# Optimization experiments

Measured on AMD Instinct MI355X. Metric: run time of the kernel, lower is better.

## Reference

```python
import jax, jax.numpy as jnp
import numpy as np

N = 100_000      # total nodes in batched graph
NE = 800_000     # total edges
G = 1_000        # number of graphs in batch
V_DIM = 128      # node feat dim (== H_DIM, required by GRUCell usage)
E_DIM = 64       # edge feat dim
H_DIM = 128      # hidden dim
K_HEAD = 4       # multi-scale interaction heads


def _leaky(x):
    return jnp.where(x >= 0, x, 0.1 * x)


def _gru_cell(x, h, Wih, Whh, bih, bhh):
    # torch nn.GRUCell math; Wih/Whh stored as [in, 3*h] with (r,z,n) chunk order
    gi = x @ Wih + bih
    gh = h @ Whh + bhh
    ir, iz, inn = jnp.split(gi, 3, axis=-1)
    hr, hz, hn = jnp.split(gh, 3, axis=-1)
    r = jax.nn.sigmoid(ir + hr)
    z = jax.nn.sigmoid(iz + hz)
    n = jnp.tanh(inn + r * hn)
    return (1.0 - z) * n + z * h


def setup_inputs() -> dict:
    key = jax.random.key(0)
    ks = iter(jax.random.split(key, 48))
    def rn(shape, scale=0.05):
        return (jax.random.normal(next(ks), shape) * scale).astype(jnp.float32)
    inp = {}
    inp["v"] = rn((N, V_DIM), 1.0)
    inp["e"] = rn((NE, E_DIM), 1.0)
    inp["s"] = rn((G, V_DIM), 1.0)
    inp["edge_src"] = jax.random.randint(next(ks), (NE,), 0, N)
    inp["edge_dst"] = jax.random.randint(next(ks), (NE,), 0, N)
    inp["node_graph"] = jnp.repeat(jnp.arange(G), N // G)  # sorted segment ids
    # top-level linears (stored [in, out])
    inp["A_w"] = rn((V_DIM, H_DIM)); inp["A_b"] = rn((H_DIM,))
    inp["mA_w"] = rn((K_HEAD, V_DIM, H_DIM)); inp["mA_b"] = rn((K_HEAD, H_DIM))
    inp["mB_w"] = rn((K_HEAD, V_DIM, H_DIM)); inp["mB_b"] = rn((K_HEAD, H_DIM))
    inp["mC_w"] = rn((K_HEAD, H_DIM)); inp["mC_b"] = rn((K_HEAD,))
    inp["mD_w"] = rn((K_HEAD, V_DIM, H_DIM)); inp["mD_b"] = rn((K_HEAD, H_DIM))
    inp["B_w"] = rn((H_DIM * K_HEAD, H_DIM)); inp["B_b"] = rn((H_DIM,))
    inp["C_w"] = rn((V_DIM, H_DIM)); inp["C_b"] = rn((H_DIM,))
    inp["K_w"] = rn((E_DIM, H_DIM)); inp["K_b"] = rn((H_DIM,))
    inp["E_w"] = rn((H_DIM + V_DIM, H_DIM)); inp["E_b"] = rn((H_DIM,))
    for pfx in ("gm", "gs"):
        inp[pfx + "_A_w"] = rn((H_DIM, H_DIM)); inp[pfx + "_A_b"] = rn((H_DIM,))
        inp[pfx + "_B_w"] = rn((H_DIM, H_DIM)); inp[pfx + "_B_b"] = rn((H_DIM,))
        inp[pfx + "_Wih"] = rn((H_DIM, 3 * H_DIM)); inp[pfx + "_Whh"] = rn((H_DIM, 3 * H_DIM))
        inp[pfx + "_bih"] = rn((3 * H_DIM,)); inp[pfx + "_bhh"] = rn((3 * H_DIM,))
    return inp


def reference(v, e, s, edge_src, edge_dst, node_graph,
              A_w, A_b, mA_w, mA_b, mB_w, mB_b, mC_w, mC_b, mD_w, mD_b,
              B_w, B_b, C_w, C_b, K_w, K_b, E_w, E_b,
              gm_A_w, gm_A_b, gm_B_w, gm_B_b, gm_Wih, gm_Whh, gm_bih, gm_bhh,
              gs_A_w, gs_A_b, gs_B_w, gs_B_b, gs_Wih, gs_Whh, gs_bih, gs_bhh):
    # super -> super
    s2s = jnp.tanh(s @ A_w + A_b)                                       # [G,H]
    # multi-head node->super attention pooling (Multi_scale_interaction)
    d_node = jnp.tanh(jnp.einsum('nv,kvh->knh', v, mA_w) + mA_b[:, None, :])     # [K,N,H]
    d_super = jnp.tanh(jnp.einsum('gv,kvh->kgh', s, mB_w) + mB_b[:, None, :])    # [K,G,H]
    a = jnp.einsum('knh,kh->nk', d_node * d_super[:, node_graph, :], mC_w) + mC_b[None, :]  # [N,K]
    a_max = jax.ops.segment_max(a, node_graph, num_segments=G, indices_are_sorted=True)
    a_exp = jnp.exp(a - a_max[node_graph])
    denom = jax.ops.segment_sum(a_exp, node_graph, num_segments=G, indices_are_sorted=True)
    attn = a_exp / denom[node_graph]                                    # per-graph softmax, [N,K]
    d_v = jnp.einsum('nv,kvh->nkh', v, mD_w) + mD_b[None, :, :]         # [N,K,H]
    pooled = jax.ops.segment_sum(d_v * attn[:, :, None], node_graph, num_segments=G,
                                 indices_are_sorted=True)               # [G,K,H]
    m2s = jnp.tanh(pooled.reshape(G, K_HEAD * H_DIM) @ B_w + B_b)       # [G,H]
    # super -> node broadcast
    s2m = jnp.tanh(s @ C_w + C_b)[node_graph]                           # [N,H]
    # edge-wise message: leaky_relu(K(e) * v_src) summed into destination node
    ve = _leaky((e @ K_w + K_b) * v[edge_src])                          # [E,H]
    sve = jax.ops.segment_sum(ve, edge_dst, num_segments=N)             # [N,H]
    m2m = _leaky(jnp.concatenate([sve, v], axis=1) @ E_w + E_b)         # [N,H]
    # adaptive GRU gate: node update
    z_m = jax.nn.sigmoid(m2m @ gm_A_w + gm_A_b + s2m @ gm_B_w + gm_B_b)
    h_m = z_m * s2m + (1.0 - z_m) * m2m
    update_v = _gru_cell(v, h_m, gm_Wih, gm_Whh, gm_bih, gm_bhh)
    # adaptive GRU gate: supernode update
    z_s = jax.nn.sigmoid(s2s @ gs_A_w + gs_A_b + m2s @ gs_B_w + gs_B_b)
    h_s = z_s * m2s + (1.0 - z_s) * s2s
    update_s = _gru_cell(s, h_s, gs_Wih, gs_Whh, gs_bih, gs_bhh)
    return (update_v, update_s)
```

## Files before the change

kernel.cpp:

```cpp
#include <hip/hip_runtime.h>

#define NN   100000
#define NEDG 800000
#define NG   1000
#define HD   128
#define EDIM 64

typedef unsigned short u16;
typedef __bf16 bf16x8 __attribute__((ext_vector_type(8)));
typedef float f32x4 __attribute__((ext_vector_type(4)));

#define MFMA16(a, b, c) __builtin_amdgcn_mfma_f32_16x16x32_bf16(a, b, c, 0, 0, 0)

#define WS_E    0
#define WS_GA   4096
#define WS_WIH  6144
#define WS_WHH  12288
#define WS_MA0  18432
#define WS_KW   26624
#define WS_LANES 27648

#define BF(base, NTT, ks, nt, lane) \
    (*(const bf16x8*)(wsw + (size_t)((base) + (((ks) * (NTT) + (nt)) * 64 + (lane))) * 8))

__device__ __forceinline__ float sigmoidf_(float x) { return 1.0f / (1.0f + __expf(-x)); }
__device__ __forceinline__ float tanhf_(float x) {
    float ax = fabsf(x);
    float e  = __expf(-2.0f * ax);
    float t  = (1.0f - e) / (1.0f + e);
    return copysignf(t, x);
}
__device__ __forceinline__ float leaky_(float x) { return x >= 0.f ? x : 0.1f * x; }
__device__ __forceinline__ u16 f2bf(float x) {
    union { float f; unsigned u; } c; c.f = x;
    unsigned r = c.u + 0x7FFF + ((c.u >> 16) & 1);
    return (u16)(r >> 16);
}

__device__ __forceinline__ void stg4(u16* lds, int P, int r, int c0, float4 v4) {
    int byteoff = (c0 << 1) ^ ((r & 7) << 4);
    u16* p = lds + r * P + (byteoff >> 1);
    p[0] = f2bf(v4.x); p[1] = f2bf(v4.y); p[2] = f2bf(v4.z); p[3] = f2bf(v4.w);
}
__device__ __forceinline__ void stg1(u16* lds, int P, int r, int c, u16 val) {
    int byteoff = (c << 1) ^ ((r & 7) << 4);
    lds[r * P + (byteoff >> 1)] = val;
}
__device__ __forceinline__ bf16x8 ldA(const u16* lds, int P, int r, int ks, int hi) {
    int byteoff = (ks * 64 + (hi << 4)) ^ ((r & 7) << 4);
    return *(const bf16x8*)(lds + r * P + (byteoff >> 1));
}

__global__ __launch_bounds__(256) void wconv(
    const float* __restrict__ E_w, const float* __restrict__ gmA_w,
    const float* __restrict__ Wih, const float* __restrict__ Whh,
    const float* __restrict__ mA_w, const float* __restrict__ K_w,
    u16* __restrict__ dst)
{
    int t = blockIdx.x * 256 + threadIdx.x;
    if (t >= WS_LANES) return;
    const float* W; int N; int local;
    if (t < 4096)       { W = E_w;  N = 128; local = t; }
    else if (t < 6144)  { W = gmA_w; N = 128; local = t - 4096; }
    else if (t < 12288) { W = Wih;  N = 384; local = t - 6144; }
    else if (t < 18432) { W = Whh;  N = 384; local = t - 12288; }
    else if (t < 26624) { int k = (t - 18432) >> 11; W = mA_w + k * 128 * 128; N = 128; local = (t - 18432) & 2047; }
    else                { W = K_w;  N = 128; local = t - 26624; }
    int lane = local & 63;
    int fid  = local >> 6;
    int NT = N >> 4;
    int ks = fid / NT, nt = fid - ks * NT;
    int krow = ks * 32 + ((lane >> 4) << 3);
    int col  = nt * 16 + (lane & 15);
    u16* d = dst + (size_t)t * 8;
    #pragma unroll
    for (int j = 0; j < 8; j++) d[j] = f2bf(W[(size_t)(krow + j) * N + col]);
}

__global__ __launch_bounds__(256) void k_hist(const int* __restrict__ edst, int* __restrict__ cnt) {
    int i = blockIdx.x * 256 + threadIdx.x;
    if (i < NEDG) atomicAdd(&cnt[edst[i]], 1);
}

__global__ __launch_bounds__(256) void k_scan1(const int* __restrict__ cnt,
                                               int* __restrict__ excl, int* __restrict__ bsum) {
    __shared__ int sd[256];
    int t = threadIdx.x, b = blockIdx.x;
    int base = b * 1024 + t * 4;
    int v0 = (base + 0 < NN) ? cnt[base + 0] : 0;
    int v1 = (base + 1 < NN) ? cnt[base + 1] : 0;
    int v2 = (base + 2 < NN) ? cnt[base + 2] : 0;
    int v3 = (base + 3 < NN) ? cnt[base + 3] : 0;
    int s = v0 + v1 + v2 + v3;
    sd[t] = s;
    __syncthreads();
    for (int off = 1; off < 256; off <<= 1) {
        int x = (t >= off) ? sd[t - off] : 0;
        __syncthreads();
        sd[t] += x;
        __syncthreads();
    }
    int incl = sd[t];
    int ex = incl - s;
    if (base + 0 < NN) excl[base + 0] = ex;
    if (base + 1 < NN) excl[base + 1] = ex + v0;
    if (base + 2 < NN) excl[base + 2] = ex + v0 + v1;
    if (base + 3 < NN) excl[base + 3] = ex + v0 + v1 + v2;
    if (t == 255) bsum[b] = incl;
}

#define NSCB 98
__global__ void k_scan2(int* __restrict__ bsum) {
    if (threadIdx.x == 0 && blockIdx.x == 0) {
        int run = 0;
        for (int i = 0; i < NSCB; i++) { int t = bsum[i]; bsum[i] = run; run += t; }
    }
}

__global__ __launch_bounds__(256) void k_scan3(const int* __restrict__ excl,
                                               const int* __restrict__ bsum, int* __restrict__ start) {
    int i = blockIdx.x * 256 + threadIdx.x;
    if (i < NN) start[i] = excl[i] + bsum[i >> 10];
}

__global__ __launch_bounds__(256) void k_scatter(const int* __restrict__ edst,
                                                 int* __restrict__ start, int* __restrict__ perm) {
    int i = blockIdx.x * 256 + threadIdx.x;
    if (i < NEDG) {
        int pos = atomicAdd(&start[edst[i]], 1);
        perm[pos] = i;
    }
}

__global__ __launch_bounds__(128) void k1_graph(
    const float* __restrict__ s,
    const float* __restrict__ A_w, const float* __restrict__ A_b,
    const float* __restrict__ mB_w, const float* __restrict__ mB_b,
    const float* __restrict__ mC_w,
    const float* __restrict__ C_w, const float* __restrict__ C_b,
    const float* __restrict__ gmB_w, const float* __restrict__ gmA_b, const float* __restrict__ gmB_b,
    float* __restrict__ s2s, float* __restrict__ wkg,
    float* __restrict__ s2m_tab, float* __restrict__ t2)
{
    __shared__ float sm[HD];
    __shared__ float sm2[HD];
    const int g = blockIdx.x, t = threadIdx.x;
    sm[t] = s[g * HD + t];
    __syncthreads();
    {
        float a = 0.f;
        #pragma unroll 8
        for (int i = 0; i < HD; i++) a = fmaf(sm[i], A_w[i * HD + t], a);
        s2s[g * HD + t] = tanhf_(a + A_b[t]);
    }
    for (int k = 0; k < 4; k++) {
        float a = 0.f;
        const float* W = mB_w + k * HD * HD;
        #pragma unroll 8
        for (int i = 0; i < HD; i++) a = fmaf(sm[i], W[i * HD + t], a);
        float d = tanhf_(a + mB_b[k * HD + t]);
        wkg[(k * NG + g) * HD + t] = d * mC_w[k * HD + t];
    }
    float s2m;
    {
        float a = 0.f;
        #pragma unroll 8
        for (int i = 0; i < HD; i++) a = fmaf(sm[i], C_w[i * HD + t], a);
        s2m = tanhf_(a + C_b[t]);
        s2m_tab[g * HD + t] = s2m;
    }
    sm2[t] = s2m;
    __syncthreads();
    {
        float a = 0.f;
        #pragma unroll 8
        for (int i = 0; i < HD; i++) a = fmaf(sm2[i], gmB_w[i * HD + t], a);
        t2[g * HD + t] = a + gmA_b[t] + gmB_b[t];
    }
}

__global__ __launch_bounds__(256) void k2_ascore(
    const float* __restrict__ v, const int* __restrict__ ngr,
    const u16* __restrict__ wsw,
    const float* __restrict__ mA_b, const float* __restrict__ mC_b,
    const float* __restrict__ wkg,
    float* __restrict__ aexp, float* __restrict__ denom)
{
    __shared__ u16 VT[64 * 128];
    const int tid = threadIdx.x;
    const int n0 = blockIdx.x * 64;
    #pragma unroll
    for (int l = 0; l < 8; l++) {
        int i = tid + 256 * l;
        int r = i >> 5, c0 = (i & 31) << 2;
        int node = n0 + r;
        float4 vv = (node < NN) ? *(const float4*)(v + (size_t)node * HD + c0)
                                : make_float4(0.f, 0.f, 0.f, 0.f);
        stg4(VT, 128, r, c0, vv);
    }
    __syncthreads();
    const int lane = tid & 63, w = tid >> 6;
    const int l15 = lane & 15, hi = lane >> 4;
    const int rbase = w * 16;
    bf16x8 av[4];
    #pragma unroll
    for (int ks = 0; ks < 4; ks++) av[ks] = ldA(VT, 128, rbase + l15, ks, hi);
    int gq[4], nodeq[4];
    #pragma unroll
    for (int q = 0; q < 4; q++) {
        int nd = n0 + rbase + hi * 4 + q;
        nodeq[q] = nd;
        gq[q] = ngr[min(nd, NN - 1)];
    }
    for (int k = 0; k < 4; k++) {
        float rs[4] = {0.f, 0.f, 0.f, 0.f};
        const float* bias = mA_b + k * HD;
        #pragma unroll
        for (int nt = 0; nt < 8; nt++) {
            f32x4 acc = {0.f, 0.f, 0.f, 0.f};
            #pragma unroll
            for (int ks = 0; ks < 4; ks++)
                acc = MFMA16(av[ks], BF(WS_MA0 + k * 2048, 8, ks, nt, lane), acc);
            int col = nt * 16 + l15;
            float bb = bias[col];
            #pragma unroll
            for (int q = 0; q < 4; q++)
                rs[q] += tanhf_(acc[q] + bb) * wkg[((size_t)k * NG + gq[q]) * HD + col];
        }
        #pragma unroll
        for (int q = 0; q < 4; q++) {
            float x = rs[q];
            x += __shfl_xor(x, 1); x += __shfl_xor(x, 2);
            x += __shfl_xor(x, 4); x += __shfl_xor(x, 8);
            if (l15 == 0 && nodeq[q] < NN) {
                float ev = __expf(x + mC_b[k]);
                aexp[(size_t)nodeq[q] * 4 + k] = ev;
                atomicAdd(&denom[gq[q] * 4 + k], ev);
            }
        }
    }
}

__global__ __launch_bounds__(256) void k3_edge_sorted(
    const float* __restrict__ e, const float* __restrict__ v,
    const int* __restrict__ esrc, const int* __restrict__ edst,
    const int* __restrict__ perm,
    const u16* __restrict__ wsw, const float* __restrict__ K_b,
    float* __restrict__ sve)
{
    __shared__ u16 ET[64 * 64];
    __shared__ int pid[64];
    const int tid = threadIdx.x;
    const int e0 = blockIdx.x * 64;
    if (tid < 64) pid[tid] = perm[e0 + tid];
    __syncthreads();
    #pragma unroll
    for (int l = 0; l < 4; l++) {
        int i = tid + 256 * l;
        int r = i >> 4, c0 = (i & 15) << 2;
        float4 ev4 = *(const float4*)(e + (size_t)pid[r] * EDIM + c0);
        stg4(ET, 64, r, c0, ev4);
    }
    __syncthreads();
    const int lane = tid & 63, w = tid >> 6;
    const int l15 = lane & 15, hi = lane >> 4;
    const int rbase = w * 16;
    bf16x8 ae[2];
    #pragma unroll
    for (int ks = 0; ks < 2; ks++) ae[ks] = ldA(ET, 64, rbase + l15, ks, hi);
    int sq[4], dq[4];
    #pragma unroll
    for (int q = 0; q < 4; q++) {
        int ei = pid[rbase + hi * 4 + q];
        sq[q] = esrc[ei]; dq[q] = edst[ei];
    }
    #pragma unroll
    for (int nt = 0; nt < 8; nt++) {
        f32x4 acc = {0.f, 0.f, 0.f, 0.f};
        acc = MFMA16(ae[0], BF(WS_KW, 8, 0, nt, lane), acc);
        acc = MFMA16(ae[1], BF(WS_KW, 8, 1, nt, lane), acc);
        int col = nt * 16 + l15;
        float kb = K_b[col];
        float vals[4];
        #pragma unroll
        for (int q = 0; q < 4; q++)
            vals[q] = leaky_((acc[q] + kb) * v[(size_t)sq[q] * HD + col]);
        float a = vals[0];
        #pragma unroll
        for (int q = 1; q < 4; q++) {
            if (dq[q] == dq[q - 1]) a += vals[q];
            else { atomicAdd(&sve[(size_t)dq[q - 1] * HD + col], a); a = vals[q]; }
        }
        atomicAdd(&sve[(size_t)dq[3] * HD + col], a);
    }
}

__global__ __launch_bounds__(256) void k3_edge_unsorted(
    const float* __restrict__ e, const float* __restrict__ v,
    const int* __restrict__ esrc, const int* __restrict__ edst,
    const u16* __restrict__ wsw, const float* __restrict__ K_b,
    float* __restrict__ sve)
{
    __shared__ u16 ET[64 * 64];
    const int tid = threadIdx.x;
    const int e0 = blockIdx.x * 64;
    #pragma unroll
    for (int l = 0; l < 4; l++) {
        int i = tid + 256 * l;
        int r = i >> 4, c0 = (i & 15) << 2;
        float4 ev4 = *(const float4*)(e + (size_t)(e0 + r) * EDIM + c0);
        stg4(ET, 64, r, c0, ev4);
    }
    __syncthreads();
    const int lane = tid & 63, w = tid >> 6;
    const int l15 = lane & 15, hi = lane >> 4;
    const int rbase = w * 16;
    bf16x8 ae[2];
    #pragma unroll
    for (int ks = 0; ks < 2; ks++) ae[ks] = ldA(ET, 64, rbase + l15, ks, hi);
    int sq[4], dq[4];
    #pragma unroll
    for (int q = 0; q < 4; q++) {
        int ei = e0 + rbase + hi * 4 + q;
        sq[q] = esrc[ei]; dq[q] = edst[ei];
    }
    #pragma unroll
    for (int nt = 0; nt < 8; nt++) {
        f32x4 acc = {0.f, 0.f, 0.f, 0.f};
        acc = MFMA16(ae[0], BF(WS_KW, 8, 0, nt, lane), acc);
        acc = MFMA16(ae[1], BF(WS_KW, 8, 1, nt, lane), acc);
        int col = nt * 16 + l15;
        float kb = K_b[col];
        #pragma unroll
        for (int q = 0; q < 4; q++) {
            float val = leaky_((acc[q] + kb) * v[(size_t)sq[q] * HD + col]);
            atomicAdd(&sve[(size_t)dq[q] * HD + col], val);
        }
    }
}

__global__ __launch_bounds__(256) void k4_vbar(
    const float* __restrict__ v, const int* __restrict__ ngr,
    const float* __restrict__ aexp, const float* __restrict__ denom,
    float* __restrict__ vbar)
{
    const int tid = threadIdx.x;
    const int d = tid & 127;
    const int hf = tid >> 7;
    const int n0 = blockIdx.x * 32 + hf * 16;
    int gcur = -1;
    float a0 = 0.f, a1 = 0.f, a2 = 0.f, a3 = 0.f;
    float4 rd = make_float4(0.f, 0.f, 0.f, 0.f);
    for (int nd = 0; nd < 16; nd++) {
        int n = n0 + nd;
        int g = ngr[n];
        if (g != gcur) {
            if (gcur >= 0) {
                atomicAdd(&vbar[(gcur * 4 + 0) * HD + d], a0);
                atomicAdd(&vbar[(gcur * 4 + 1) * HD + d], a1);
                atomicAdd(&vbar[(gcur * 4 + 2) * HD + d], a2);
                atomicAdd(&vbar[(gcur * 4 + 3) * HD + d], a3);
                a0 = a1 = a2 = a3 = 0.f;
            }
            float4 dn = *(const float4*)&denom[g * 4];
            rd = make_float4(1.f / dn.x, 1.f / dn.y, 1.f / dn.z, 1.f / dn.w);
            gcur = g;
        }
        float4 ae = *(const float4*)&aexp[n * 4];
        float vv = v[(size_t)n * HD + d];
        a0 = fmaf(ae.x * rd.x, vv, a0);
        a1 = fmaf(ae.y * rd.y, vv, a1);
        a2 = fmaf(ae.z * rd.z, vv, a2);
        a3 = fmaf(ae.w * rd.w, vv, a3);
    }
    atomicAdd(&vbar[(gcur * 4 + 0) * HD + d], a0);
    atomicAdd(&vbar[(gcur * 4 + 1) * HD + d], a1);
    atomicAdd(&vbar[(gcur * 4 + 2) * HD + d], a2);
    atomicAdd(&vbar[(gcur * 4 + 3) * HD + d], a3);
}

__global__ __launch_bounds__(128) void k5_super(
    const float* __restrict__ s, const float* __restrict__ vbar,
    const float* __restrict__ mD_w, const float* __restrict__ mD_b,
    const float* __restrict__ B_w, const float* __restrict__ B_b,
    const float* __restrict__ s2s,
    const float* __restrict__ gsA_w, const float* __restrict__ gsA_b,
    const float* __restrict__ gsB_w, const float* __restrict__ gsB_b,
    const float* __restrict__ gsWih, const float* __restrict__ gsWhh,
    const float* __restrict__ gsbih, const float* __restrict__ gsbhh,
    float* __restrict__ out_s)
{
    __shared__ float vb[4 * HD];
    __shared__ float p[4 * HD];
    __shared__ float m2s_l[HD];
    __shared__ float s2s_l[HD];
    __shared__ float hs_l[HD];
    __shared__ float srow[HD];
    const int g = blockIdx.x, t = threadIdx.x;
    #pragma unroll
    for (int l = 0; l < 4; l++) vb[t + HD * l] = vbar[(size_t)g * 4 * HD + t + HD * l];
    srow[t]  = s[g * HD + t];
    s2s_l[t] = s2s[g * HD + t];
    __syncthreads();
    for (int k = 0; k < 4; k++) {
        float a = 0.f;
        const float* W = mD_w + k * HD * HD;
        #pragma unroll 8
        for (int i = 0; i < HD; i++) a = fmaf(vb[k * HD + i], W[i * HD + t], a);
        p[k * HD + t] = a + mD_b[k * HD + t];
    }
    __syncthreads();
    float m2s;
    {
        float a = 0.f;
        #pragma unroll 8
        for (int j = 0; j < 4 * HD; j++) a = fmaf(p[j], B_w[j * HD + t], a);
        m2s = tanhf_(a + B_b[t]);
        m2s_l[t] = m2s;
    }
    __syncthreads();
    float hs;
    {
        float za = 0.f, zb = 0.f;
        #pragma unroll 8
        for (int i = 0; i < HD; i++) {
            za = fmaf(s2s_l[i], gsA_w[i * HD + t], za);
            zb = fmaf(m2s_l[i], gsB_w[i * HD + t], zb);
        }
        float z = sigmoidf_(za + gsA_b[t] + zb + gsB_b[t]);
        hs = z * m2s + (1.f - z) * s2s_l[t];
        hs_l[t] = hs;
    }
    __syncthreads();
    float gi0 = 0.f, gh0 = 0.f, gi1 = 0.f, gh1 = 0.f, gi2 = 0.f, gh2 = 0.f;
    #pragma unroll 4
    for (int i = 0; i < HD; i++) {
        float sv = srow[i], hv = hs_l[i];
        gi0 = fmaf(sv, gsWih[i * 384 + t], gi0);
        gh0 = fmaf(hv, gsWhh[i * 384 + t], gh0);
        gi1 = fmaf(sv, gsWih[i * 384 + 128 + t], gi1);
        gh1 = fmaf(hv, gsWhh[i * 384 + 128 + t], gh1);
        gi2 = fmaf(sv, gsWih[i * 384 + 256 + t], gi2);
        gh2 = fmaf(hv, gsWhh[i * 384 + 256 + t], gh2);
    }
    float r  = sigmoidf_(gi0 + gsbih[t] + gh0 + gsbhh[t]);
    float z2 = sigmoidf_(gi1 + gsbih[128 + t] + gh1 + gsbhh[128 + t]);
    float nn = tanhf_(gi2 + gsbih[256 + t] + r * (gh2 + gsbhh[256 + t]));
    out_s[g * HD + t] = (1.f - z2) * nn + z2 * hs;
}

__global__ __launch_bounds__(256) void k6_node(
    const float* __restrict__ v, const int* __restrict__ ngr,
    const float* __restrict__ sve, const u16* __restrict__ wsw,
    const float* __restrict__ E_b,
    const float* __restrict__ s2m_tab, const float* __restrict__ t2,
    const float* __restrict__ bih, const float* __restrict__ bhh,
    float* __restrict__ out_v)
{
    __shared__ u16 VT[64 * 128];
    __shared__ u16 ST[64 * 128];
    __shared__ u16 XT[64 * 128];
    const int tid = threadIdx.x;
    const int n0 = blockIdx.x * 64;
    #pragma unroll
    for (int l = 0; l < 8; l++) {
        int i = tid + 256 * l;
        int r = i >> 5, c0 = (i & 31) << 2;
        int node = n0 + r;
        float4 a = (node < NN) ? *(const float4*)(v   + (size_t)node * HD + c0) : make_float4(0.f, 0.f, 0.f, 0.f);
        float4 b = (node < NN) ? *(const float4*)(sve + (size_t)node * HD + c0) : make_float4(0.f, 0.f, 0.f, 0.f);
        stg4(VT, 128, r, c0, a);
        stg4(ST, 128, r, c0, b);
    }
    __syncthreads();
    const int lane = tid & 63, w = tid >> 6;
    const int l15 = lane & 15, hi = lane >> 4;
    const int rbase = w * 16;
    bf16x8 av[4], ax[4];
    #pragma unroll
    for (int ks = 0; ks < 4; ks++) {
        av[ks] = ldA(VT, 128, rbase + l15, ks, hi);
        ax[ks] = ldA(ST, 128, rbase + l15, ks, hi);
    }
    int gq[4], nodeq[4];
    #pragma unroll
    for (int q = 0; q < 4; q++) {
        int nd = n0 + rbase + hi * 4 + q;
        nodeq[q] = nd;
        gq[q] = ngr[min(nd, NN - 1)];
    }
    f32x4 hmf[8];
    #pragma unroll
    for (int nt = 0; nt < 8; nt++) {
        f32x4 acc = {0.f, 0.f, 0.f, 0.f};
        #pragma unroll
        for (int ks = 0; ks < 4; ks++) acc = MFMA16(ax[ks], BF(WS_E, 8, ks, nt, lane), acc);
        #pragma unroll
        for (int ks = 0; ks < 4; ks++) acc = MFMA16(av[ks], BF(WS_E, 8, 4 + ks, nt, lane), acc);
        int col = nt * 16 + l15;
        float eb = E_b[col];
        f32x4 m;
        #pragma unroll
        for (int q = 0; q < 4; q++) m[q] = leaky_(acc[q] + eb);
        hmf[nt] = m;
    }
    #pragma unroll
    for (int nt = 0; nt < 8; nt++) {
        int col = nt * 16 + l15;
        #pragma unroll
        for (int q = 0; q < 4; q++) stg1(ST, 128, rbase + hi * 4 + q, col, f2bf(hmf[nt][q]));
    }
    bf16x8 am[4];
    #pragma unroll
    for (int ks = 0; ks < 4; ks++) am[ks] = ldA(ST, 128, rbase + l15, ks, hi);
    #pragma unroll
    for (int nt = 0; nt < 8; nt++) {
        f32x4 acc = {0.f, 0.f, 0.f, 0.f};
        #pragma unroll
        for (int ks = 0; ks < 4; ks++) acc = MFMA16(am[ks], BF(WS_GA, 8, ks, nt, lane), acc);
        int col = nt * 16 + l15;
        #pragma unroll
        for (int q = 0; q < 4; q++) {
            int g = gq[q];
            float z  = sigmoidf_(acc[q] + t2[(size_t)g * HD + col]);
            float hm = z * s2m_tab[(size_t)g * HD + col] + (1.f - z) * hmf[nt][q];
            hmf[nt][q] = hm;
            stg1(XT, 128, rbase + hi * 4 + q, col, f2bf(hm));
        }
    }
    bf16x8 ah[4];
    #pragma unroll
    for (int ks = 0; ks < 4; ks++) ah[ks] = ldA(XT, 128, rbase + l15, ks, hi);
    #pragma unroll
    for (int nt = 0; nt < 8; nt++) {
        f32x4 air = {0.f,0.f,0.f,0.f}, aiz = {0.f,0.f,0.f,0.f}, ain = {0.f,0.f,0.f,0.f};
        f32x4 ahr = {0.f,0.f,0.f,0.f}, ahz = {0.f,0.f,0.f,0.f}, ahn = {0.f,0.f,0.f,0.f};
        #pragma unroll
        for (int ks = 0; ks < 4; ks++) {
            air = MFMA16(av[ks], BF(WS_WIH, 24, ks, nt,      lane), air);
            ahr = MFMA16(ah[ks], BF(WS_WHH, 24, ks, nt,      lane), ahr);
            aiz = MFMA16(av[ks], BF(WS_WIH, 24, ks, nt + 8,  lane), aiz);
            ahz = MFMA16(ah[ks], BF(WS_WHH, 24, ks, nt + 8,  lane), ahz);
            ain = MFMA16(av[ks], BF(WS_WIH, 24, ks, nt + 16, lane), ain);
            ahn = MFMA16(ah[ks], BF(WS_WHH, 24, ks, nt + 16, lane), ahn);
        }
        int col = nt * 16 + l15;
        float br  = bih[col] + bhh[col];
        float bz  = bih[HD + col] + bhh[HD + col];
        float bi3 = bih[2 * HD + col];
        float bh3 = bhh[2 * HD + col];
        #pragma unroll
        for (int q = 0; q < 4; q++) {
            float r   = sigmoidf_(air[q] + ahr[q] + br);
            float z   = sigmoidf_(aiz[q] + ahz[q] + bz);
            float nnv = tanhf_(ain[q] + bi3 + r * (ahn[q] + bh3));
            if (nodeq[q] < NN)
                out_v[(size_t)nodeq[q] * HD + col] = (1.f - z) * nnv + z * hmf[nt][q];
        }
    }
}

extern "C" void kernel_launch(void* const* d_in, const int* in_sizes, int n_in,
                              void* d_out, int out_size, void* d_ws, size_t ws_size,
                              hipStream_t stream)
{
    const float* v    = (const float*)d_in[0];
    const float* e    = (const float*)d_in[1];
    const float* s    = (const float*)d_in[2];
    const int*   esrc = (const int*)d_in[3];
    const int*   edst = (const int*)d_in[4];
    const int*   ngr  = (const int*)d_in[5];
    const float* A_w  = (const float*)d_in[6];
    const float* A_b  = (const float*)d_in[7];
    const float* mA_w = (const float*)d_in[8];
    const float* mA_b = (const float*)d_in[9];
    const float* mB_w = (const float*)d_in[10];
    const float* mB_b = (const float*)d_in[11];
    const float* mC_w = (const float*)d_in[12];
    const float* mC_b = (const float*)d_in[13];
    const float* mD_w = (const float*)d_in[14];
    const float* mD_b = (const float*)d_in[15];
    const float* B_w  = (const float*)d_in[16];
    const float* B_b  = (const float*)d_in[17];
    const float* C_w  = (const float*)d_in[18];
    const float* C_b  = (const float*)d_in[19];
    const float* K_w  = (const float*)d_in[20];
    const float* K_b  = (const float*)d_in[21];
    const float* E_w  = (const float*)d_in[22];
    const float* E_b  = (const float*)d_in[23];
    const float* gmA_w = (const float*)d_in[24];
    const float* gmA_b = (const float*)d_in[25];
    const float* gmB_w = (const float*)d_in[26];
    const float* gmB_b = (const float*)d_in[27];
    const float* gmWih = (const float*)d_in[28];
    const float* gmWhh = (const float*)d_in[29];
    const float* gmbih = (const float*)d_in[30];
    const float* gmbhh = (const float*)d_in[31];
    const float* gsA_w = (const float*)d_in[32];
    const float* gsA_b = (const float*)d_in[33];
    const float* gsB_w = (const float*)d_in[34];
    const float* gsB_b = (const float*)d_in[35];
    const float* gsWih = (const float*)d_in[36];
    const float* gsWhh = (const float*)d_in[37];
    const float* gsbih = (const float*)d_in[38];
    const float* gsbhh = (const float*)d_in[39];

    float* ws      = (float*)d_ws;
    float* sve     = ws;
    float* aexp    = sve + 12800000;
    float* denom   = aexp + 400000;
    float* wkg     = denom + 4000;
    float* s2s     = wkg + 512000;
    float* s2m_tab = s2s + 128000;
    float* t2      = s2m_tab + 128000;
    float* vbar    = t2 + 128000;
    u16*   wswz    = (u16*)(vbar + 512000);
    int*   isc     = (int*)(wswz + 221184);
    int*   cnt     = isc;
    int*   excl    = cnt + 100000;
    int*   bsum    = excl + 100000;
    int*   startp  = bsum + 128;
    int*   perm    = startp + 100000;
    const size_t NEED = ((size_t)(perm + 800000 - (int*)d_ws)) * 4;
    const bool do_sort = ws_size >= NEED;

    hipMemsetAsync(sve, 0, (size_t)12800000 * 4, stream);
    hipMemsetAsync(denom, 0, (size_t)4000 * 4, stream);
    hipMemsetAsync(vbar, 0, (size_t)512000 * 4, stream);

    float* out_v = (float*)d_out;
    float* out_s = out_v + (size_t)NN * HD;

    wconv<<<(WS_LANES + 255) / 256, 256, 0, stream>>>(E_w, gmA_w, gmWih, gmWhh, mA_w, K_w, wswz);
    k1_graph<<<NG, 128, 0, stream>>>(s, A_w, A_b, mB_w, mB_b, mC_w, C_w, C_b,
                                     gmB_w, gmA_b, gmB_b, s2s, wkg, s2m_tab, t2);
    if (do_sort) {
        hipMemsetAsync(cnt, 0, (size_t)100000 * 4, stream);
        k_hist<<<(NEDG + 255) / 256, 256, 0, stream>>>(edst, cnt);
        k_scan1<<<NSCB, 256, 0, stream>>>(cnt, excl, bsum);
        k_scan2<<<1, 64, 0, stream>>>(bsum);
        k_scan3<<<(NN + 255) / 256, 256, 0, stream>>>(excl, bsum, startp);
        k_scatter<<<(NEDG + 255) / 256, 256, 0, stream>>>(edst, startp, perm);
    }
    k2_ascore<<<(NN + 63) / 64, 256, 0, stream>>>(v, ngr, wswz, mA_b, mC_b, wkg, aexp, denom);
    if (do_sort) {
        k3_edge_sorted<<<NEDG / 64, 256, 0, stream>>>(e, v, esrc, edst, perm, wswz, K_b, sve);
    } else {
        k3_edge_unsorted<<<NEDG / 64, 256, 0, stream>>>(e, v, esrc, edst, wswz, K_b, sve);
    }
    k4_vbar<<<NN / 32, 256, 0, stream>>>(v, ngr, aexp, denom, vbar);
    k5_super<<<NG, 128, 0, stream>>>(s, vbar, mD_w, mD_b, B_w, B_b, s2s,
                                     gsA_w, gsA_b, gsB_w, gsB_b,
                                     gsWih, gsWhh, gsbih, gsbhh, out_s);
    k6_node<<<(NN + 63) / 64, 256, 0, stream>>>(v, ngr, sve, wswz, E_b, s2m_tab, t2,
                                                gmbih, gmbhh, out_v);
}
```

Before: 778.6 us.

## Process edges per destination-node block with LDS accumulation instead of global atomics

The sorted edge kernel now launches one block per 64 destination nodes and walks that block's CSR edge range. Messages are accumulated with shared-memory atomics and written to sve once, which removes the global atomics and the 51 MB memset of sve on the sorted path. The scan also emits a rowptr array for the CSR ranges. The cost is fewer blocks with uneven work (about 512 edges each, in a serial loop) and extra LDS use, which may reduce occupancy.

```diff
diff --git a/kernel.cpp b/kernel.cpp
--- a/kernel.cpp
+++ b/kernel.cpp
@@ -118,9 +118,15 @@
 }
 
 __global__ __launch_bounds__(256) void k_scan3(const int* __restrict__ excl,
-                                               const int* __restrict__ bsum, int* __restrict__ start) {
+                                               const int* __restrict__ bsum,
+                                               int* __restrict__ start, int* __restrict__ rowptr) {
     int i = blockIdx.x * 256 + threadIdx.x;
-    if (i < NN) start[i] = excl[i] + bsum[i >> 10];
+    if (i < NN) {
+        int sv = excl[i] + bsum[i >> 10];
+        start[i] = sv;
+        rowptr[i] = sv;
+    }
+    if (i == NN) rowptr[NN] = NEDG;
 }
 
 __global__ __launch_bounds__(256) void k_scatter(const int* __restrict__ edst,
@@ -241,57 +247,79 @@
     }
 }
 
-__global__ __launch_bounds__(256) void k3_edge_sorted(
+#define ACCP 132
+__global__ __launch_bounds__(256) void k3_edge_lds(
     const float* __restrict__ e, const float* __restrict__ v,
     const int* __restrict__ esrc, const int* __restrict__ edst,
-    const int* __restrict__ perm,
+    const int* __restrict__ perm, const int* __restrict__ rowptr,
     const u16* __restrict__ wsw, const float* __restrict__ K_b,
     float* __restrict__ sve)
 {
+    __shared__ float acc[64 * ACCP];
     __shared__ u16 ET[64 * 64];
     __shared__ int pid[64];
     const int tid = threadIdx.x;
-    const int e0 = blockIdx.x * 64;
-    if (tid < 64) pid[tid] = perm[e0 + tid];
-    __syncthreads();
-    #pragma unroll
-    for (int l = 0; l < 4; l++) {
+    const int n0 = blockIdx.x * 64;
+    const int r0 = rowptr[n0];
+    const int r1 = rowptr[min(n0 + 64, NN)];
+    #pragma unroll
+    for (int l = 0; l < 8; l++) {
         int i = tid + 256 * l;
-        int r = i >> 4, c0 = (i & 15) << 2;
-        float4 ev4 = *(const float4*)(e + (size_t)pid[r] * EDIM + c0);
-        stg4(ET, 64, r, c0, ev4);
-    }
-    __syncthreads();
+        int row = i >> 5, c0 = (i & 31) << 2;
+        *(float4*)&acc[row * ACCP + c0] = make_float4(0.f, 0.f, 0.f, 0.f);
+    }
     const int lane = tid & 63, w = tid >> 6;
     const int l15 = lane & 15, hi = lane >> 4;
     const int rbase = w * 16;
-    bf16x8 ae[2];
-    #pragma unroll
-    for (int ks = 0; ks < 2; ks++) ae[ks] = ldA(ET, 64, rbase + l15, ks, hi);
-    int sq[4], dq[4];
-    #pragma unroll
-    for (int q = 0; q < 4; q++) {
-        int ei = pid[rbase + hi * 4 + q];
-        sq[q] = esrc[ei]; dq[q] = edst[ei];
-    }
-    #pragma unroll
-    for (int nt = 0; nt < 8; nt++) {
-        f32x4 acc = {0.f, 0.f, 0.f, 0.f};
-        acc = MFMA16(ae[0], BF(WS_KW, 8, 0, nt, lane), acc);
-        acc = MFMA16(ae[1], BF(WS_KW, 8, 1, nt, lane), acc);
-        int col = nt * 16 + l15;
-        float kb = K_b[col];
-        float vals[4];
-        #pragma unroll
-        for (int q = 0; q < 4; q++)
-            vals[q] = leaky_((acc[q] + kb) * v[(size_t)sq[q] * HD + col]);
-        float a = vals[0];
-        #pragma unroll
-        for (int q = 1; q < 4; q++) {
-            if (dq[q] == dq[q - 1]) a += vals[q];
-            else { atomicAdd(&sve[(size_t)dq[q - 1] * HD + col], a); a = vals[q]; }
-        }
-        atomicAdd(&sve[(size_t)dq[3] * HD + col], a);
+    const float kb_ = K_b[0];
+    (void)kb_;
+    for (int c = r0; c < r1; c += 64) {
+        __syncthreads();
+        if (tid < 64) pid[tid] = perm[min(c + tid, r1 - 1)];
+        __syncthreads();
+        #pragma unroll
+        for (int l = 0; l < 4; l++) {
+            int i = tid + 256 * l;
+            int r = i >> 4, c0 = (i & 15) << 2;
+            float4 ev4 = *(const float4*)(e + (size_t)pid[r] * EDIM + c0);
+            stg4(ET, 64, r, c0, ev4);
+        }
+        __syncthreads();
+        bf16x8 ae[2];
+        #pragma unroll
+        for (int ks = 0; ks < 2; ks++) ae[ks] = ldA(ET, 64, rbase + l15, ks, hi);
+        int sq[4], dl[4];
+        bool ok[4];
+        #pragma unroll
+        for (int q = 0; q < 4; q++) {
+            int r = rbase + hi * 4 + q;
+            ok[q] = (c + r < r1);
+            int ei = pid[r];
+            sq[q] = esrc[ei];
+            dl[q] = ok[q] ? (edst[ei] - n0) : 0;
+        }
+        #pragma unroll
+        for (int nt = 0; nt < 8; nt++) {
+            f32x4 a2 = {0.f, 0.f, 0.f, 0.f};
+            a2 = MFMA16(ae[0], BF(WS_KW, 8, 0, nt, lane), a2);
+            a2 = MFMA16(ae[1], BF(WS_KW, 8, 1, nt, lane), a2);
+            int col = nt * 16 + l15;
+            float kb = K_b[col];
+            #pragma unroll
+            for (int q = 0; q < 4; q++) {
+                float val = leaky_((a2[q] + kb) * v[(size_t)sq[q] * HD + col]);
+                if (ok[q]) atomicAdd(&acc[dl[q] * ACCP + col], val);
+            }
+        }
+    }
+    __syncthreads();
+    #pragma unroll
+    for (int l = 0; l < 8; l++) {
+        int i = tid + 256 * l;
+        int row = i >> 5, c0 = (i & 31) << 2;
+        int node = n0 + row;
+        if (node < NN)
+            *(float4*)(sve + (size_t)node * HD + c0) = *(const float4*)&acc[row * ACCP + c0];
     }
 }
 
@@ -620,13 +648,14 @@
     int*   excl    = cnt + 100000;
     int*   bsum    = excl + 100000;
     int*   startp  = bsum + 128;
-    int*   perm    = startp + 100000;
+    int*   rowptr  = startp + 100000;
+    int*   perm    = rowptr + 100032;
     const size_t NEED = ((size_t)(perm + 800000 - (int*)d_ws)) * 4;
     const bool do_sort = ws_size >= NEED;
 
-    hipMemsetAsync(sve, 0, (size_t)12800000 * 4, stream);
     hipMemsetAsync(denom, 0, (size_t)4000 * 4, stream);
     hipMemsetAsync(vbar, 0, (size_t)512000 * 4, stream);
+    if (!do_sort) hipMemsetAsync(sve, 0, (size_t)12800000 * 4, stream);
 
     float* out_v = (float*)d_out;
     float* out_s = out_v + (size_t)NN * HD;
@@ -639,12 +668,13 @@
         k_hist<<<(NEDG + 255) / 256, 256, 0, stream>>>(edst, cnt);
         k_scan1<<<NSCB, 256, 0, stream>>>(cnt, excl, bsum);
         k_scan2<<<1, 64, 0, stream>>>(bsum);
-        k_scan3<<<(NN + 255) / 256, 256, 0, stream>>>(excl, bsum, startp);
+        k_scan3<<<(NN + 256) / 256, 256, 0, stream>>>(excl, bsum, startp, rowptr);
         k_scatter<<<(NEDG + 255) / 256, 256, 0, stream>>>(edst, startp, perm);
     }
     k2_ascore<<<(NN + 63) / 64, 256, 0, stream>>>(v, ngr, wswz, mA_b, mC_b, wkg, aexp, denom);
     if (do_sort) {
-        k3_edge_sorted<<<NEDG / 64, 256, 0, stream>>>(e, v, esrc, edst, perm, wswz, K_b, sve);
+        k3_edge_lds<<<(NN + 63) / 64, 256, 0, stream>>>(e, v, esrc, edst, perm, rowptr,
+                                                        wswz, K_b, sve);
     } else {
         k3_edge_unsorted<<<NEDG / 64, 256, 0, stream>>>(e, v, esrc, edst, wswz, K_b, sve);
     }
```

After: 1.176 ms. 1.51x slower.

## Write edge messages in CSR order as bf16 then segment-sum per node

Applied to the files above, without the earlier changes.

Splits the edge message stage into two kernels. The first computes each edge's message with coalesced edge loads and writes it as bf16 to its sorted destination slot. The second does an atomic-free segmented sum per destination node using the CSR row pointers and writes sve directly, which removes the 51 MB zero-fill of sve. The cost is roughly 200 MB of extra bf16 round-trip traffic, bf16 rounding of each message before the sum, and a path that only runs when the workspace is large enough.

```diff
diff --git a/kernel.cpp b/kernel.cpp
--- a/kernel.cpp
+++ b/kernel.cpp
@@ -9,6 +9,7 @@
 typedef unsigned short u16;
 typedef __bf16 bf16x8 __attribute__((ext_vector_type(8)));
 typedef float f32x4 __attribute__((ext_vector_type(4)));
+typedef u16 u16x8 __attribute__((ext_vector_type(8)));
 
 #define MFMA16(a, b, c) __builtin_amdgcn_mfma_f32_16x16x32_bf16(a, b, c, 0, 0, 0)
 
@@ -35,6 +36,9 @@
     union { float f; unsigned u; } c; c.f = x;
     unsigned r = c.u + 0x7FFF + ((c.u >> 16) & 1);
     return (u16)(r >> 16);
+}
+__device__ __forceinline__ float bfbits2f(unsigned hw) {
+    union { unsigned u; float f; } c; c.u = hw << 16; return c.f;
 }
 
 __device__ __forceinline__ void stg4(u16* lds, int P, int r, int c0, float4 v4) {
@@ -118,17 +122,26 @@
 }
 
 __global__ __launch_bounds__(256) void k_scan3(const int* __restrict__ excl,
-                                               const int* __restrict__ bsum, int* __restrict__ start) {
+                                               const int* __restrict__ bsum,
+                                               int* __restrict__ start, int* __restrict__ rowptr) {
     int i = blockIdx.x * 256 + threadIdx.x;
-    if (i < NN) start[i] = excl[i] + bsum[i >> 10];
+    if (i < NN) {
+        int sv = excl[i] + bsum[i >> 10];
+        start[i] = sv;
+        rowptr[i] = sv;
+    }
+    if (i == NN) rowptr[NN] = NEDG;
 }
 
 __global__ __launch_bounds__(256) void k_scatter(const int* __restrict__ edst,
-                                                 int* __restrict__ start, int* __restrict__ perm) {
+                                                 int* __restrict__ start,
+                                                 int* __restrict__ perm,
+                                                 int* __restrict__ outpos) {
     int i = blockIdx.x * 256 + threadIdx.x;
     if (i < NEDG) {
         int pos = atomicAdd(&start[edst[i]], 1);
         perm[pos] = i;
+        outpos[i] = pos;
     }
 }
 
@@ -239,6 +252,86 @@
             }
         }
     }
+}
+
+__global__ __launch_bounds__(256) void k3a_edge(
+    const float* __restrict__ e, const float* __restrict__ v,
+    const int* __restrict__ esrc, const int* __restrict__ outpos,
+    const u16* __restrict__ wsw, const float* __restrict__ K_b,
+    u16* __restrict__ vesrt)
+{
+    __shared__ u16 ET[64 * 64];
+    __shared__ u16 OUT[64 * 128];
+    __shared__ int posa[64];
+    const int tid = threadIdx.x;
+    const int e0 = blockIdx.x * 64;
+    if (tid < 64) posa[tid] = outpos[e0 + tid];
+    #pragma unroll
+    for (int l = 0; l < 4; l++) {
+        int i = tid + 256 * l;
+        int r = i >> 4, c0 = (i & 15) << 2;
+        float4 ev4 = *(const float4*)(e + (size_t)(e0 + r) * EDIM + c0);
+        stg4(ET, 64, r, c0, ev4);
+    }
+    __syncthreads();
+    const int lane = tid & 63, w = tid >> 6;
+    const int l15 = lane & 15, hi = lane >> 4;
+    const int rbase = w * 16;
+    bf16x8 ae[2];
+    #pragma unroll
+    for (int ks = 0; ks < 2; ks++) ae[ks] = ldA(ET, 64, rbase + l15, ks, hi);
+    int sq[4];
+    #pragma unroll
+    for (int q = 0; q < 4; q++) sq[q] = esrc[e0 + rbase + hi * 4 + q];
+    #pragma unroll
+    for (int nt = 0; nt < 8; nt++) {
+        f32x4 acc = {0.f, 0.f, 0.f, 0.f};
+        acc = MFMA16(ae[0], BF(WS_KW, 8, 0, nt, lane), acc);
+        acc = MFMA16(ae[1], BF(WS_KW, 8, 1, nt, lane), acc);
+        int col = nt * 16 + l15;
+        float kb = K_b[col];
+        #pragma unroll
+        for (int q = 0; q < 4; q++) {
+            float val = leaky_((acc[q] + kb) * v[(size_t)sq[q] * HD + col]);
+            stg1(OUT, 128, rbase + hi * 4 + q, col, f2bf(val));
+        }
+    }
+    __syncthreads();
+    #pragma unroll
+    for (int l = 0; l < 4; l++) {
+        int i = tid + 256 * l;
+        int r = i >> 4, seg = i & 15;
+        int segp = seg ^ (r & 7);
+        u16x8 val = *(const u16x8*)&OUT[r * 128 + segp * 8];
+        *(u16x8*)(vesrt + (size_t)posa[r] * HD + ((segp ^ (r & 7)) * 8)) = val;
+    }
+}
+
+__global__ __launch_bounds__(256) void k3b_segsum(
+    const u16* __restrict__ vesrt, const int* __restrict__ rowptr,
+    float* __restrict__ sve)
+{
+    const int wid = threadIdx.x >> 6, lane = threadIdx.x & 63;
+    const int n = blockIdx.x * 4 + wid;
+    if (n >= NN) return;
+    const int r0 = rowptr[n], r1 = rowptr[n + 1];
+    const unsigned* base = (const unsigned*)vesrt;
+    float a0 = 0.f, a1 = 0.f;
+    int r = r0;
+    for (; r + 4 <= r1; r += 4) {
+        unsigned x0 = base[(size_t)(r + 0) * 64 + lane];
+        unsigned x1 = base[(size_t)(r + 1) * 64 + lane];
+        unsigned x2 = base[(size_t)(r + 2) * 64 + lane];
+        unsigned x3 = base[(size_t)(r + 3) * 64 + lane];
+        a0 += bfbits2f(x0 & 0xffff) + bfbits2f(x1 & 0xffff) + bfbits2f(x2 & 0xffff) + bfbits2f(x3 & 0xffff);
+        a1 += bfbits2f(x0 >> 16) + bfbits2f(x1 >> 16) + bfbits2f(x2 >> 16) + bfbits2f(x3 >> 16);
+    }
+    for (; r < r1; r++) {
+        unsigned x = base[(size_t)r * 64 + lane];
+        a0 += bfbits2f(x & 0xffff);
+        a1 += bfbits2f(x >> 16);
+    }
+    *(float2*)(sve + (size_t)n * HD + lane * 2) = make_float2(a0, a1);
 }
 
 __global__ __launch_bounds__(256) void k3_edge_sorted(
@@ -620,13 +713,18 @@
     int*   excl    = cnt + 100000;
     int*   bsum    = excl + 100000;
     int*   startp  = bsum + 128;
-    int*   perm    = startp + 100000;
-    const size_t NEED = ((size_t)(perm + 800000 - (int*)d_ws)) * 4;
-    const bool do_sort = ws_size >= NEED;
-
-    hipMemsetAsync(sve, 0, (size_t)12800000 * 4, stream);
+    int*   rowptr  = startp + 100000;
+    int*   perm    = rowptr + 100032;
+    int*   outpos  = perm + 800000;
+    u16*   vesrt   = (u16*)(outpos + 800000);
+    const size_t NEED_SORT = ((size_t)((int*)vesrt - (int*)d_ws)) * 4;
+    const size_t NEED_FULL = NEED_SORT + (size_t)102400000 * 2;
+    const bool do_sort = ws_size >= NEED_SORT;
+    const bool do_full = ws_size >= NEED_FULL;
+
     hipMemsetAsync(denom, 0, (size_t)4000 * 4, stream);
     hipMemsetAsync(vbar, 0, (size_t)512000 * 4, stream);
+    if (!do_full) hipMemsetAsync(sve, 0, (size_t)12800000 * 4, stream);
 
     float* out_v = (float*)d_out;
     float* out_s = out_v + (size_t)NN * HD;
@@ -639,11 +737,14 @@
         k_hist<<<(NEDG + 255) / 256, 256, 0, stream>>>(edst, cnt);
         k_scan1<<<NSCB, 256, 0, stream>>>(cnt, excl, bsum);
         k_scan2<<<1, 64, 0, stream>>>(bsum);
-        k_scan3<<<(NN + 255) / 256, 256, 0, stream>>>(excl, bsum, startp);
-        k_scatter<<<(NEDG + 255) / 256, 256, 0, stream>>>(edst, startp, perm);
+        k_scan3<<<(NN + 256) / 256, 256, 0, stream>>>(excl, bsum, startp, rowptr);
+        k_scatter<<<(NEDG + 255) / 256, 256, 0, stream>>>(edst, startp, perm, outpos);
     }
     k2_ascore<<<(NN + 63) / 64, 256, 0, stream>>>(v, ngr, wswz, mA_b, mC_b, wkg, aexp, denom);
-    if (do_sort) {
+    if (do_full) {
+        k3a_edge<<<NEDG / 64, 256, 0, stream>>>(e, v, esrc, outpos, wswz, K_b, vesrt);
+        k3b_segsum<<<(NN + 3) / 4, 256, 0, stream>>>(vesrt, rowptr, sve);
+    } else if (do_sort) {
         k3_edge_sorted<<<NEDG / 64, 256, 0, stream>>>(e, v, esrc, edst, perm, wswz, K_b, sve);
     } else {
         k3_edge_unsorted<<<NEDG / 64, 256, 0, stream>>>(e, v, esrc, edst, wswz, K_b, sve);
```

Measured after the change: 734.7 us. 5.6% less time.

## Merge sorted edge messages in LDS per block and load node rows directly

Applied to the files above, without the earlier changes.

The sorted edge kernel now writes all 64 edge messages for a block into shared memory and has 128 threads walk the rows per column, merging runs of equal destination before issuing atomics. This cuts the global atomic count compared with merging only within groups of four rows. The node kernel drops its block-wide LDS staging of v and sve and loads MFMA A-fragments straight from global memory, converting them to bf16 in registers. It also keeps intermediates as packed bf16 in a per-wave LDS tile, which reduces LDS use and barriers but rounds the h_m blend input and GRU carry to bf16.

```diff
diff --git a/kernel.cpp b/kernel.cpp
--- a/kernel.cpp
+++ b/kernel.cpp
@@ -9,6 +9,8 @@
 typedef unsigned short u16;
 typedef __bf16 bf16x8 __attribute__((ext_vector_type(8)));
 typedef float f32x4 __attribute__((ext_vector_type(4)));
+typedef u16 u16x8 __attribute__((ext_vector_type(8)));
+typedef unsigned u32x4 __attribute__((ext_vector_type(4)));
 
 #define MFMA16(a, b, c) __builtin_amdgcn_mfma_f32_16x16x32_bf16(a, b, c, 0, 0, 0)
 
@@ -35,6 +37,22 @@
     union { float f; unsigned u; } c; c.f = x;
     unsigned r = c.u + 0x7FFF + ((c.u >> 16) & 1);
     return (u16)(r >> 16);
+}
+__device__ __forceinline__ float bfbits2f(unsigned hw) {
+    union { unsigned u; float f; } c; c.u = hw << 16; return c.f;
+}
+__device__ __forceinline__ unsigned pack2bf(float lo, float hi) {
+    return (unsigned)f2bf(lo) | ((unsigned)f2bf(hi) << 16);
+}
+__device__ __forceinline__ bf16x8 mk8(const float* __restrict__ p) {
+    float4 a = *(const float4*)p;
+    float4 b = *(const float4*)(p + 4);
+    union { u32x4 u; bf16x8 v; } c;
+    c.u[0] = pack2bf(a.x, a.y);
+    c.u[1] = pack2bf(a.z, a.w);
+    c.u[2] = pack2bf(b.x, b.y);
+    c.u[3] = pack2bf(b.z, b.w);
+    return c.v;
 }
 
 __device__ __forceinline__ void stg4(u16* lds, int P, int r, int c0, float4 v4) {
@@ -118,13 +136,15 @@
 }
 
 __global__ __launch_bounds__(256) void k_scan3(const int* __restrict__ excl,
-                                               const int* __restrict__ bsum, int* __restrict__ start) {
+                                               const int* __restrict__ bsum,
+                                               int* __restrict__ start) {
     int i = blockIdx.x * 256 + threadIdx.x;
     if (i < NN) start[i] = excl[i] + bsum[i >> 10];
 }
 
 __global__ __launch_bounds__(256) void k_scatter(const int* __restrict__ edst,
-                                                 int* __restrict__ start, int* __restrict__ perm) {
+                                                 int* __restrict__ start,
+                                                 int* __restrict__ perm) {
     int i = blockIdx.x * 256 + threadIdx.x;
     if (i < NEDG) {
         int pos = atomicAdd(&start[edst[i]], 1);
@@ -241,7 +261,8 @@
     }
 }
 
-__global__ __launch_bounds__(256) void k3_edge_sorted(
+#define OP 129
+__global__ __launch_bounds__(256) void k3_merge(
     const float* __restrict__ e, const float* __restrict__ v,
     const int* __restrict__ esrc, const int* __restrict__ edst,
     const int* __restrict__ perm,
@@ -249,10 +270,16 @@
     float* __restrict__ sve)
 {
     __shared__ u16 ET[64 * 64];
+    __shared__ float OUTF[64 * OP];
     __shared__ int pid[64];
+    __shared__ int dsta[64];
     const int tid = threadIdx.x;
     const int e0 = blockIdx.x * 64;
-    if (tid < 64) pid[tid] = perm[e0 + tid];
+    if (tid < 64) {
+        int p = perm[e0 + tid];
+        pid[tid] = p;
+        dsta[tid] = edst[p];
+    }
     __syncthreads();
     #pragma unroll
     for (int l = 0; l < 4; l++) {
@@ -268,12 +295,9 @@
     bf16x8 ae[2];
     #pragma unroll
     for (int ks = 0; ks < 2; ks++) ae[ks] = ldA(ET, 64, rbase + l15, ks, hi);
-    int sq[4], dq[4];
-    #pragma unroll
-    for (int q = 0; q < 4; q++) {
-        int ei = pid[rbase + hi * 4 + q];
-        sq[q] = esrc[ei]; dq[q] = edst[ei];
-    }
+    int sq[4];
+    #pragma unroll
+    for (int q = 0; q < 4; q++) sq[q] = esrc[pid[rbase + hi * 4 + q]];
     #pragma unroll
     for (int nt = 0; nt < 8; nt++) {
         f32x4 acc = {0.f, 0.f, 0.f, 0.f};
@@ -281,17 +305,28 @@
         acc = MFMA16(ae[1], BF(WS_KW, 8, 1, nt, lane), acc);
         int col = nt * 16 + l15;
         float kb = K_b[col];
-        float vals[4];
-        #pragma unroll
-        for (int q = 0; q < 4; q++)
-            vals[q] = leaky_((acc[q] + kb) * v[(size_t)sq[q] * HD + col]);
-        float a = vals[0];
-        #pragma unroll
-        for (int q = 1; q < 4; q++) {
-            if (dq[q] == dq[q - 1]) a += vals[q];
-            else { atomicAdd(&sve[(size_t)dq[q - 1] * HD + col], a); a = vals[q]; }
-        }
-        atomicAdd(&sve[(size_t)dq[3] * HD + col], a);
+        #pragma unroll
+        for (int q = 0; q < 4; q++) {
+            float val = leaky_((acc[q] + kb) * v[(size_t)sq[q] * HD + col]);
+            OUTF[(rbase + hi * 4 + q) * OP + col] = val;
+        }
+    }
+    __syncthreads();
+    if (tid < 128) {
+        const int c = tid;
+        int dcur = dsta[0];
+        float acc = OUTF[c];
+        #pragma unroll 4
+        for (int r = 1; r < 64; r++) {
+            int d = dsta[r];
+            float x = OUTF[r * OP + c];
+            if (d == dcur) acc += x;
+            else {
+                atomicAdd(&sve[(size_t)dcur * HD + c], acc);
+                dcur = d; acc = x;
+            }
+        }
+        atomicAdd(&sve[(size_t)dcur * HD + c], acc);
     }
 }
 
@@ -449,7 +484,7 @@
     out_s[g * HD + t] = (1.f - z2) * nn + z2 * hs;
 }
 
-__global__ __launch_bounds__(256) void k6_node(
+__global__ __launch_bounds__(256) void k6_node_sve(
     const float* __restrict__ v, const int* __restrict__ ngr,
     const float* __restrict__ sve, const u16* __restrict__ wsw,
     const float* __restrict__ E_b,
@@ -457,39 +492,27 @@
     const float* __restrict__ bih, const float* __restrict__ bhh,
     float* __restrict__ out_v)
 {
-    __shared__ u16 VT[64 * 128];
-    __shared__ u16 ST[64 * 128];
-    __shared__ u16 XT[64 * 128];
+    __shared__ u16 TT[4][16 * 128];
     const int tid = threadIdx.x;
-    const int n0 = blockIdx.x * 64;
-    #pragma unroll
-    for (int l = 0; l < 8; l++) {
-        int i = tid + 256 * l;
-        int r = i >> 5, c0 = (i & 31) << 2;
-        int node = n0 + r;
-        float4 a = (node < NN) ? *(const float4*)(v   + (size_t)node * HD + c0) : make_float4(0.f, 0.f, 0.f, 0.f);
-        float4 b = (node < NN) ? *(const float4*)(sve + (size_t)node * HD + c0) : make_float4(0.f, 0.f, 0.f, 0.f);
-        stg4(VT, 128, r, c0, a);
-        stg4(ST, 128, r, c0, b);
-    }
-    __syncthreads();
     const int lane = tid & 63, w = tid >> 6;
     const int l15 = lane & 15, hi = lane >> 4;
-    const int rbase = w * 16;
+    const int n0 = blockIdx.x * 64 + w * 16;
+    u16* T = TT[w];
+    const int arow = min(n0 + l15, NN - 1);
     bf16x8 av[4], ax[4];
     #pragma unroll
     for (int ks = 0; ks < 4; ks++) {
-        av[ks] = ldA(VT, 128, rbase + l15, ks, hi);
-        ax[ks] = ldA(ST, 128, rbase + l15, ks, hi);
+        av[ks] = mk8(v   + (size_t)arow * HD + ks * 32 + hi * 8);
+        ax[ks] = mk8(sve + (size_t)arow * HD + ks * 32 + hi * 8);
     }
     int gq[4], nodeq[4];
     #pragma unroll
     for (int q = 0; q < 4; q++) {
-        int nd = n0 + rbase + hi * 4 + q;
+        int nd = n0 + hi * 4 + q;
         nodeq[q] = nd;
         gq[q] = ngr[min(nd, NN - 1)];
     }
-    f32x4 hmf[8];
+    unsigned m2mp[8][2];
     #pragma unroll
     for (int nt = 0; nt < 8; nt++) {
         f32x4 acc = {0.f, 0.f, 0.f, 0.f};
@@ -497,40 +520,46 @@
         for (int ks = 0; ks < 4; ks++) acc = MFMA16(ax[ks], BF(WS_E, 8, ks, nt, lane), acc);
         #pragma unroll
         for (int ks = 0; ks < 4; ks++) acc = MFMA16(av[ks], BF(WS_E, 8, 4 + ks, nt, lane), acc);
+        float eb = E_b[nt * 16 + l15];
+        float m0 = leaky_(acc[0] + eb), m1 = leaky_(acc[1] + eb);
+        float m2 = leaky_(acc[2] + eb), m3 = leaky_(acc[3] + eb);
+        m2mp[nt][0] = pack2bf(m0, m1);
+        m2mp[nt][1] = pack2bf(m2, m3);
         int col = nt * 16 + l15;
-        float eb = E_b[col];
-        f32x4 m;
-        #pragma unroll
-        for (int q = 0; q < 4; q++) m[q] = leaky_(acc[q] + eb);
-        hmf[nt] = m;
-    }
-    #pragma unroll
-    for (int nt = 0; nt < 8; nt++) {
-        int col = nt * 16 + l15;
-        #pragma unroll
-        for (int q = 0; q < 4; q++) stg1(ST, 128, rbase + hi * 4 + q, col, f2bf(hmf[nt][q]));
+        stg1(T, 128, hi * 4 + 0, col, (u16)(m2mp[nt][0] & 0xffff));
+        stg1(T, 128, hi * 4 + 1, col, (u16)(m2mp[nt][0] >> 16));
+        stg1(T, 128, hi * 4 + 2, col, (u16)(m2mp[nt][1] & 0xffff));
+        stg1(T, 128, hi * 4 + 3, col, (u16)(m2mp[nt][1] >> 16));
     }
     bf16x8 am[4];
     #pragma unroll
-    for (int ks = 0; ks < 4; ks++) am[ks] = ldA(ST, 128, rbase + l15, ks, hi);
+    for (int ks = 0; ks < 4; ks++) am[ks] = ldA(T, 128, l15, ks, hi);
+    unsigned hmp[8][2];
     #pragma unroll
     for (int nt = 0; nt < 8; nt++) {
         f32x4 acc = {0.f, 0.f, 0.f, 0.f};
         #pragma unroll
         for (int ks = 0; ks < 4; ks++) acc = MFMA16(am[ks], BF(WS_GA, 8, ks, nt, lane), acc);
         int col = nt * 16 + l15;
+        float m2mq[4] = { bfbits2f(m2mp[nt][0] & 0xffff), bfbits2f(m2mp[nt][0] >> 16),
+                          bfbits2f(m2mp[nt][1] & 0xffff), bfbits2f(m2mp[nt][1] >> 16) };
+        float hm[4];
         #pragma unroll
         for (int q = 0; q < 4; q++) {
             int g = gq[q];
-            float z  = sigmoidf_(acc[q] + t2[(size_t)g * HD + col]);
-            float hm = z * s2m_tab[(size_t)g * HD + col] + (1.f - z) * hmf[nt][q];
-            hmf[nt][q] = hm;
-            stg1(XT, 128, rbase + hi * 4 + q, col, f2bf(hm));
-        }
+            float z = sigmoidf_(acc[q] + t2[(size_t)g * HD + col]);
+            hm[q] = z * s2m_tab[(size_t)g * HD + col] + (1.f - z) * m2mq[q];
+        }
+        hmp[nt][0] = pack2bf(hm[0], hm[1]);
+        hmp[nt][1] = pack2bf(hm[2], hm[3]);
+        stg1(T, 128, hi * 4 + 0, col, (u16)(hmp[nt][0] & 0xffff));
+        stg1(T, 128, hi * 4 + 1, col, (u16)(hmp[nt][0] >> 16));
+        stg1(T, 128, hi * 4 + 2, col, (u16)(hmp[nt][1] & 0xffff));
+        stg1(T, 128, hi * 4 + 3, col, (u16)(hmp[nt][1] >> 16));
     }
     bf16x8 ah[4];
     #pragma unroll
-    for (int ks = 0; ks < 4; ks++) ah[ks] = ldA(XT, 128, rbase + l15, ks, hi);
+    for (int ks = 0; ks < 4; ks++) ah[ks] = ldA(T, 128, l15, ks, hi);
     #pragma unroll
     for (int nt = 0; nt < 8; nt++) {
         f32x4 air = {0.f,0.f,0.f,0.f}, aiz = {0.f,0.f,0.f,0.f}, ain = {0.f,0.f,0.f,0.f};
@@ -549,13 +578,15 @@
         float bz  = bih[HD + col] + bhh[HD + col];
         float bi3 = bih[2 * HD + col];
         float bh3 = bhh[2 * HD + col];
+        float hmq[4] = { bfbits2f(hmp[nt][0] & 0xffff), bfbits2f(hmp[nt][0] >> 16),
+                         bfbits2f(hmp[nt][1] & 0xffff), bfbits2f(hmp[nt][1] >> 16) };
         #pragma unroll
         for (int q = 0; q < 4; q++) {
             float r   = sigmoidf_(air[q] + ahr[q] + br);
             float z   = sigmoidf_(aiz[q] + ahz[q] + bz);
             float nnv = tanhf_(ain[q] + bi3 + r * (ahn[q] + bh3));
             if (nodeq[q] < NN)
-                out_v[(size_t)nodeq[q] * HD + col] = (1.f - z) * nnv + z * hmf[nt][q];
+                out_v[(size_t)nodeq[q] * HD + col] = (1.f - z) * nnv + z * hmq[q];
         }
     }
 }
@@ -621,8 +652,8 @@
     int*   bsum    = excl + 100000;
     int*   startp  = bsum + 128;
     int*   perm    = startp + 100000;
-    const size_t NEED = ((size_t)(perm + 800000 - (int*)d_ws)) * 4;
-    const bool do_sort = ws_size >= NEED;
+    const size_t NEED_SORT = ((size_t)(perm + 800000 - (int*)d_ws)) * 4;
+    const bool do_sort = ws_size >= NEED_SORT;
 
     hipMemsetAsync(sve, 0, (size_t)12800000 * 4, stream);
     hipMemsetAsync(denom, 0, (size_t)4000 * 4, stream);
@@ -644,7 +675,7 @@
     }
     k2_ascore<<<(NN + 63) / 64, 256, 0, stream>>>(v, ngr, wswz, mA_b, mC_b, wkg, aexp, denom);
     if (do_sort) {
-        k3_edge_sorted<<<NEDG / 64, 256, 0, stream>>>(e, v, esrc, edst, perm, wswz, K_b, sve);
+        k3_merge<<<NEDG / 64, 256, 0, stream>>>(e, v, esrc, edst, perm, wswz, K_b, sve);
     } else {
         k3_edge_unsorted<<<NEDG / 64, 256, 0, stream>>>(e, v, esrc, edst, wswz, K_b, sve);
     }
@@ -652,6 +683,6 @@
     k5_super<<<NG, 128, 0, stream>>>(s, vbar, mD_w, mD_b, B_w, B_b, s2s,
                                      gsA_w, gsA_b, gsB_w, gsB_b,
                                      gsWih, gsWhh, gsbih, gsbhh, out_s);
-    k6_node<<<(NN + 63) / 64, 256, 0, stream>>>(v, ngr, sve, wswz, E_b, s2m_tab, t2,
-                                                gmbih, gmbhh, out_v);
-}
+    k6_node_sve<<<(NN + 63) / 64, 256, 0, stream>>>(v, ngr, sve, wswz, E_b, s2m_tab, t2,
+                                                    gmbih, gmbhh, out_v);
+}
```

Result: faster. 727.3 us (-6.6%).
